# Optimization experiments

Measured on AMD Instinct MI355X. Metric: run time of the kernel, lower is better.

Reference implementation:

```python
import jax, jax.numpy as jnp
import numpy as np

D_MODEL = 1024
NHEAD = 16
HEAD_DIM = D_MODEL // NHEAD
NEG = -1e9
LN_EPS = 1e-5


def setup_inputs() -> dict:
    key = jax.random.key(0)
    ks = jax.random.split(key, 12)
    B, S, D = 2, 2048, D_MODEL
    scale = 1.0 / np.sqrt(D)
    inp = {
        "x": jax.random.normal(ks[0], (B, S, D), jnp.float32),
        "mask": jax.random.randint(ks[1], (B, S), 0, 2, jnp.int32),
        "wq": jax.random.normal(ks[2], (D, D), jnp.float32) * scale,
        "bq": jnp.zeros((D,), jnp.float32),
        "wk": jax.random.normal(ks[3], (D, D), jnp.float32) * scale,
        "bk": jnp.zeros((D,), jnp.float32),
        "wv": jax.random.normal(ks[4], (D, D), jnp.float32) * scale,
        "bv": jnp.zeros((D,), jnp.float32),
        "wo": jax.random.normal(ks[5], (D, D), jnp.float32) * scale,
        "bo": jnp.zeros((D,), jnp.float32),
        "attn_bias": jax.random.normal(ks[6], (1, NHEAD, 1, 1), jnp.float32) * 0.02,
        "ln_g": jnp.ones((D,), jnp.float32),
        "ln_b": jnp.zeros((D,), jnp.float32),
    }
    return inp


def _layer_norm(x, g, b):
    mu = jnp.mean(x, axis=-1, keepdims=True)
    var = jnp.var(x, axis=-1, keepdims=True)
    return (x - mu) * jax.lax.rsqrt(var + LN_EPS) * g + b


def reference(x, mask, wq, bq, wk, bk, wv, bv, wo, bo, attn_bias, ln_g, ln_b):
    B, S, D = x.shape
    H, Hd = NHEAD, HEAD_DIM
    # QKV projections -> [B, H, S, Hd]
    q = (x @ wq + bq).reshape(B, S, H, Hd).transpose(0, 2, 1, 3)
    k = (x @ wk + bk).reshape(B, S, H, Hd).transpose(0, 2, 1, 3)
    v = (x @ wv + bv).reshape(B, S, H, Hd).transpose(0, 2, 1, 3)
    # Scores [B, H, S, S] with per-head scalar bias
    scores = jnp.einsum("bhsd,bhtd->bhst", q, k) / jnp.sqrt(jnp.float32(Hd))
    scores = scores + attn_bias
    # mask [B,S] -> [B,1,1,S]; masked_fill where mask == 0
    m = (mask[:, None, None, :] == 0)
    scores = jnp.where(m, jnp.float32(NEG), scores)
    attn = jax.nn.softmax(scores, axis=-1)  # dropout = identity (eval)
    out = jnp.einsum("bhst,bhtd->bhsd", attn, v)
    out = out.transpose(0, 2, 1, 3).reshape(B, S, D)
    out = out @ wo + bo
    return _layer_norm(x + out, ln_g, ln_b)
```

## Files before the change

kernel.cpp:

```cpp
#include <hip/hip_runtime.h>

typedef __attribute__((ext_vector_type(8))) short short8;
typedef __attribute__((ext_vector_type(4))) float f32x4;
typedef __attribute__((ext_vector_type(16))) float f32x16;
typedef __attribute__((ext_vector_type(4))) unsigned short us4;

#define DEV __device__ __forceinline__

#define GLD16(gp, lp) __builtin_amdgcn_global_load_lds( \
    (const __attribute__((address_space(1))) void*)(gp), \
    (__attribute__((address_space(3))) void*)(lp), 16, 0, 0)

DEV unsigned short f2bf(float f) {
    union { float f; unsigned u; } v; v.f = f;
    unsigned r = v.u + 0x7fffu + ((v.u >> 16) & 1u);
    return (unsigned short)(r >> 16);
}

DEV float bf2f(unsigned short u) {
    union { unsigned u; float f; } v; v.u = (unsigned)u << 16;
    return v.f;
}

DEV unsigned short f2h(float f) {
    union { _Float16 h; unsigned short u; } v; v.h = (_Float16)f; return v.u;
}

DEV float h2f(unsigned short u) {
    union { _Float16 h; unsigned short u; } v; v.u = u; return (float)v.h;
}

DEV unsigned cvtpk(float lo, float hi) {
    unsigned r;
    asm("v_cvt_pk_bf16_f32 %0, %1, %2" : "=v"(r) : "v"(lo), "v"(hi));
    return r;
}

DEV float fexp2(float x) {
#if __has_builtin(__builtin_amdgcn_exp2f)
    return __builtin_amdgcn_exp2f(x);
#else
    return __expf(x * 0.69314718056f);
#endif
}

__global__ __launch_bounds__(256) void k_prep(const float* __restrict__ x, unsigned short* __restrict__ xb,
                                              const float* __restrict__ wq, const float* __restrict__ wk,
                                              const float* __restrict__ wv, const float* __restrict__ wo,
                                              unsigned short* __restrict__ wt) {
    __shared__ float tile[32][33];
    const int id = blockIdx.x, tid = threadIdx.x;
    if (id < 4096) {
        int i = id * 256 + tid;
        float4 v = ((const float4*)x)[i];
        us4 o = { f2bf(v.x), f2bf(v.y), f2bf(v.z), f2bf(v.w) };
        ((us4*)xb)[i] = o;
        return;
    }
    const int t = (id - 4096) & 1023, z = (id - 4096) >> 10;
    const float* src = (z == 0) ? wq : (z == 1) ? wk : (z == 2) ? wv : wo;
    unsigned short* dst = wt + (size_t)z * (1u << 20);
    const int n0 = (t & 31) * 32, k0 = (t >> 5) * 32;
    const int tx = tid & 31, ty = tid >> 5;
#pragma unroll
    for (int i = 0; i < 4; ++i)
        tile[ty + i * 8][tx] = src[(size_t)(k0 + ty + i * 8) * 1024 + n0 + tx];
    __syncthreads();
#pragma unroll
    for (int i = 0; i < 4; ++i)
        dst[(size_t)(n0 + ty + i * 8) * 1024 + k0 + tx] = f2bf(tile[tx][ty + i * 8]);
}

__global__ __launch_bounds__(256) void k_gemm_qkv(const unsigned short* __restrict__ A,
                                                  const unsigned short* __restrict__ Wt,
                                                  const float* __restrict__ bq,
                                                  const float* __restrict__ bk,
                                                  const float* __restrict__ bv,
                                                  const int* __restrict__ mask,
                                                  unsigned short* __restrict__ Qo,
                                                  unsigned short* __restrict__ Ko,
                                                  unsigned short* __restrict__ Vo,
                                                  float qscale) {
    __shared__ unsigned short lA[2][128 * 32];
    __shared__ unsigned short lB[2][3][64 * 32];
    const int id = blockIdx.x;
    const int m0 = ((id & 7) * 4 + ((id >> 3) & 3)) * 128;
    const int n0 = (id >> 5) * 64;
    const int tid = threadIdx.x;
    const int lane = tid & 63;
    const int w = tid >> 6, wm = w >> 1, wn = w & 1;

    const int arow0 = tid >> 2, acl = tid & 3;
    const int arow1 = (tid + 256) >> 2;
    const int brow = tid >> 2;
    const unsigned short* agp0 = A + (size_t)(m0 + arow0) * 1024 + acl * 8;
    const unsigned short* agp1 = A + (size_t)(m0 + arow1) * 1024 + acl * 8;
    const unsigned short* bgp[3];
#pragma unroll
    for (int z = 0; z < 3; ++z)
        bgp[z] = Wt + ((size_t)z << 20) + (size_t)(n0 + brow) * 1024 + acl * 8;
    const int apc0 = ((arow0 << 2) | (acl ^ ((arow0 >> 1) & 3))) * 8;
    const int apc1 = ((arow1 << 2) | (acl ^ ((arow1 >> 1) & 3))) * 8;
    const int bpc  = ((brow  << 2) | (acl ^ ((brow  >> 1) & 3))) * 8;

    int ach[4], bch[2];
#pragma unroll
    for (int mt = 0; mt < 4; ++mt) {
        int row = wm * 64 + mt * 16 + (lane & 15);
        ach[mt] = ((row << 2) | ((lane >> 4) ^ ((row >> 1) & 3))) * 8;
    }
#pragma unroll
    for (int nt = 0; nt < 2; ++nt) {
        int row = wn * 32 + nt * 16 + (lane & 15);
        bch[nt] = ((row << 2) | ((lane >> 4) ^ ((row >> 1) & 3))) * 8;
    }

    f32x4 acc[3][4][2] = {};
    short8 ra0 = *(const short8*)agp0;
    short8 ra1 = *(const short8*)agp1;
    short8 rb[3];
#pragma unroll
    for (int z = 0; z < 3; ++z) rb[z] = *(const short8*)bgp[z];

    for (int t = 0; t < 32; ++t) {
        unsigned short* sA = lA[t & 1];
        *(short8*)(sA + apc0) = ra0;
        *(short8*)(sA + apc1) = ra1;
#pragma unroll
        for (int z = 0; z < 3; ++z)
            *(short8*)(lB[t & 1][z] + bpc) = rb[z];
        if (t < 31) {
            ra0 = *(const short8*)(agp0 + (t + 1) * 32);
            ra1 = *(const short8*)(agp1 + (t + 1) * 32);
#pragma unroll
            for (int z = 0; z < 3; ++z) rb[z] = *(const short8*)(bgp[z] + (t + 1) * 32);
        }
        __syncthreads();
        short8 af[4], bf[3][2];
#pragma unroll
        for (int mt = 0; mt < 4; ++mt) af[mt] = *(const short8*)(sA + ach[mt]);
#pragma unroll
        for (int z = 0; z < 3; ++z)
#pragma unroll
            for (int nt = 0; nt < 2; ++nt) bf[z][nt] = *(const short8*)(lB[t & 1][z] + bch[nt]);
#pragma unroll
        for (int z = 0; z < 3; ++z)
#pragma unroll
            for (int mt = 0; mt < 4; ++mt)
#pragma unroll
                for (int nt = 0; nt < 2; ++nt)
                    acc[z][mt][nt] = __builtin_amdgcn_mfma_f32_16x16x32_bf16(af[mt], bf[z][nt], acc[z][mt][nt], 0, 0, 0);
    }

#pragma unroll
    for (int z = 0; z < 3; ++z) {
        const float* bias = (z == 0) ? bq : (z == 1) ? bk : bv;
        const float scl = (z == 0) ? qscale : 1.0f;
        unsigned short* outp = (z == 0) ? Qo : (z == 1) ? Ko : Vo;
#pragma unroll
        for (int nt = 0; nt < 2; ++nt) {
            const int col = n0 + wn * 32 + nt * 16 + (lane & 15);
            const float bvv = bias[col];
            const int h = col >> 6, hd = col & 63;
#pragma unroll
            for (int mt = 0; mt < 4; ++mt) {
#pragma unroll
                for (int r = 0; r < 4; ++r) {
                    const int row = m0 + wm * 64 + mt * 16 + (lane >> 4) * 4 + r;
                    const int b = row >> 11, s = row & 2047;
                    float v = (acc[z][mt][nt][r] + bvv) * scl;
                    if (z == 2) {
                        v *= (mask[(size_t)b * 2048 + s] ? 1.0f : 0.0f);
                        outp[(size_t)((b * 16 + h) * 64 + hd) * 2048 + s] = f2bf(v);
                    } else {
                        outp[(size_t)((b * 16 + h) * 2048 + s) * 64 + hd] = f2bf(v);
                    }
                }
            }
        }
    }
}

__global__ __launch_bounds__(256) void k_gemm_o(const unsigned short* __restrict__ A,
                                                const unsigned short* __restrict__ Wt,
                                                const float* __restrict__ bias,
                                                unsigned short* __restrict__ out) {
    __shared__ unsigned short lA[2][128 * 32];
    __shared__ unsigned short lB[2][128 * 32];
    const int id = blockIdx.x;
    const int kk = id >> 3;
    const int m0 = ((id & 7) * 4 + (kk >> 3)) * 128;
    const int n0 = (kk & 7) * 128;
    const int tid = threadIdx.x;
    const int lane = tid & 63;
    const int w = tid >> 6, wm = w >> 1, wn = w & 1;

    const int arow0 = tid >> 2, acl = tid & 3;
    const int arow1 = arow0 + 64;
    const unsigned short* agp0 = A + (size_t)(m0 + arow0) * 1024 + acl * 8;
    const unsigned short* agp1 = A + (size_t)(m0 + arow1) * 1024 + acl * 8;
    const unsigned short* bgp0 = Wt + (size_t)(n0 + arow0) * 1024 + acl * 8;
    const unsigned short* bgp1 = Wt + (size_t)(n0 + arow1) * 1024 + acl * 8;
    const int apc0 = ((arow0 << 2) | (acl ^ ((arow0 >> 1) & 3))) * 8;
    const int apc1 = ((arow1 << 2) | (acl ^ ((arow1 >> 1) & 3))) * 8;

    int ach[4], bch[4];
#pragma unroll
    for (int mt = 0; mt < 4; ++mt) {
        int row = wm * 64 + mt * 16 + (lane & 15);
        ach[mt] = ((row << 2) | ((lane >> 4) ^ ((row >> 1) & 3))) * 8;
    }
#pragma unroll
    for (int nt = 0; nt < 4; ++nt) {
        int row = wn * 64 + nt * 16 + (lane & 15);
        bch[nt] = ((row << 2) | ((lane >> 4) ^ ((row >> 1) & 3))) * 8;
    }

    f32x4 acc[4][4] = {};
    short8 ra0 = *(const short8*)agp0;
    short8 ra1 = *(const short8*)agp1;
    short8 rb0 = *(const short8*)bgp0;
    short8 rb1 = *(const short8*)bgp1;

    for (int t = 0; t < 32; ++t) {
        unsigned short* sA = lA[t & 1];
        unsigned short* sB = lB[t & 1];
        *(short8*)(sA + apc0) = ra0;
        *(short8*)(sA + apc1) = ra1;
        *(short8*)(sB + apc0) = rb0;
        *(short8*)(sB + apc1) = rb1;
        if (t < 31) {
            ra0 = *(const short8*)(agp0 + (t + 1) * 32);
            ra1 = *(const short8*)(agp1 + (t + 1) * 32);
            rb0 = *(const short8*)(bgp0 + (t + 1) * 32);
            rb1 = *(const short8*)(bgp1 + (t + 1) * 32);
        }
        __syncthreads();
        short8 af[4], bf[4];
#pragma unroll
        for (int mt = 0; mt < 4; ++mt) af[mt] = *(const short8*)(sA + ach[mt]);
#pragma unroll
        for (int nt = 0; nt < 4; ++nt) bf[nt] = *(const short8*)(sB + bch[nt]);
#pragma unroll
        for (int mt = 0; mt < 4; ++mt)
#pragma unroll
            for (int nt = 0; nt < 4; ++nt)
                acc[mt][nt] = __builtin_amdgcn_mfma_f32_16x16x32_bf16(af[mt], bf[nt], acc[mt][nt], 0, 0, 0);
    }

#pragma unroll
    for (int nt = 0; nt < 4; ++nt) {
        const int col = n0 + wn * 64 + nt * 16 + (lane & 15);
        const float bv = bias[col];
#pragma unroll
        for (int mt = 0; mt < 4; ++mt)
#pragma unroll
            for (int r = 0; r < 4; ++r) {
                const int row = m0 + wm * 64 + mt * 16 + (lane >> 4) * 4 + r;
                out[(size_t)row * 1024 + col] = f2bf(acc[mt][nt][r] + bv);
            }
    }
}

__global__ __launch_bounds__(256, 3) void k_attn(const unsigned short* __restrict__ Qb,
                                                 const unsigned short* __restrict__ Kb,
                                                 const unsigned short* __restrict__ Vt,
                                                 const int* __restrict__ mask,
                                                 unsigned short* __restrict__ po0,
                                                 unsigned short* __restrict__ po1,
                                                 unsigned short* __restrict__ po2,
                                                 unsigned short* __restrict__ po3,
                                                 float* __restrict__ lp) {
    __shared__ unsigned short ksm[3 * 4096];
    __shared__ unsigned short vsm[3 * 4096];
    __shared__ unsigned short mv[512];
    const int id = blockIdx.x;
    const int xcd = id & 7, slot = id >> 3;
    const int half = slot & 3, qt = (slot >> 2) & 15, bh = xcd * 4 + (slot >> 6);
    const int b = bh >> 4, h = bh & 15;
    const int tid = threadIdx.x, l = tid & 63, w = tid >> 6;
    const int q = l & 31, hi = l >> 5;

    {
        int2 m = ((const int2*)(mask + b * 2048 + half * 512))[tid];
        ((unsigned*)mv)[tid] = (m.x ? 0x3F80u : 0u) | ((m.y ? 0x3F80u : 0u) << 16);
    }
    asm volatile("s_waitcnt lgkmcnt(0)" ::: "memory");

    const size_t bhS = (size_t)bh * 2048;
    const unsigned short* Kbh = Kb + (bhS + half * 512) * 64;
    const unsigned short* Vbh = Vt + (size_t)bh * 64 * 2048;
    const int q0 = qt * 128 + w * 32;

    const int srow = l >> 3;
    const int sxor = 8 * ((l & 7) ^ ((l >> 3) & 7));
    const unsigned short* Ksrc = Kbh + (size_t)(w * 16 + srow) * 64 + sxor;
    const unsigned short* Vsrc = Vbh + (size_t)(w * 16 + srow) * 2048 + half * 512 + sxor;
    unsigned short* lk0 = ksm + w * 1024;
    unsigned short* lv0 = vsm + w * 1024;

#define STAGE(kt_, buf_) { \
    const unsigned short* gk = Ksrc + (size_t)(kt_) * 4096; \
    const unsigned short* gv = Vsrc + (kt_) * 64; \
    unsigned short* lk = lk0 + (buf_) * 4096; \
    unsigned short* lv = lv0 + (buf_) * 4096; \
    GLD16(gk, lk); GLD16(gk + 512, lk + 512); \
    GLD16(gv, lv); GLD16(gv + 16384, lv + 512); }

    int kro[2][4], vro[2][2][2];
#pragma unroll
    for (int sub = 0; sub < 2; ++sub) {
#pragma unroll
        for (int db = 0; db < 4; ++db) {
            int key = q + sub * 32;
            kro[sub][db] = key * 128 + ((db * 32 + hi * 16) ^ ((key & 7) << 4));
        }
#pragma unroll
        for (int kg = 0; kg < 2; ++kg)
#pragma unroll
            for (int dh = 0; dh < 2; ++dh) {
                int row = q + dh * 32;
                vro[sub][kg][dh] = row * 128 + ((sub * 64 + kg * 32 + hi * 16) ^ ((row & 7) << 4));
            }
    }

    short8 qf[4];
#pragma unroll
    for (int db = 0; db < 4; ++db)
        qf[db] = *(const short8*)(Qb + (bhS + q0 + q) * 64 + db * 16 + hi * 8);

    f32x16 o0 = {}, o1 = {}, ol = {};

    STAGE(0, 0);
    STAGE(1, 1);

#pragma unroll
    for (int kt = 0; kt < 8; ++kt) {
        const int cur = kt % 3;
        if (kt < 7) {
            asm volatile("s_waitcnt vmcnt(4)" ::: "memory");
        } else {
            asm volatile("s_waitcnt vmcnt(0)" ::: "memory");
        }
        __builtin_amdgcn_s_barrier();
        if (kt < 6) STAGE(kt + 2, (kt + 2) % 3);
        __builtin_amdgcn_sched_barrier(0);
        const char* kb = (const char*)(ksm + cur * 4096);
        const char* vb = (const char*)(vsm + cur * 4096);
#pragma unroll
        for (int sub = 0; sub < 2; ++sub) {
            short8 kf0 = *(const short8*)(kb + kro[sub][0]);
            short8 kf1 = *(const short8*)(kb + kro[sub][1]);
            short8 kf2 = *(const short8*)(kb + kro[sub][2]);
            short8 kf3 = *(const short8*)(kb + kro[sub][3]);
            f32x16 sa = {};
            __builtin_amdgcn_s_setprio(1);
            sa = __builtin_amdgcn_mfma_f32_32x32x16_bf16(kf0, qf[0], sa, 0, 0, 0);
            sa = __builtin_amdgcn_mfma_f32_32x32x16_bf16(kf1, qf[1], sa, 0, 0, 0);
            sa = __builtin_amdgcn_mfma_f32_32x32x16_bf16(kf2, qf[2], sa, 0, 0, 0);
            sa = __builtin_amdgcn_mfma_f32_32x32x16_bf16(kf3, qf[3], sa, 0, 0, 0);
            __builtin_amdgcn_s_setprio(0);
            float p[16];
#pragma unroll
            for (int r = 0; r < 16; ++r) p[r] = fexp2(sa[r]);
            union { unsigned u[4]; short8 s8; } af[2];
#pragma unroll
            for (int kg = 0; kg < 2; ++kg) {
                unsigned P0 = cvtpk(p[kg * 8 + 0], p[kg * 8 + 1]);
                unsigned P1 = cvtpk(p[kg * 8 + 2], p[kg * 8 + 3]);
                unsigned P2 = cvtpk(p[kg * 8 + 4], p[kg * 8 + 5]);
                unsigned P3 = cvtpk(p[kg * 8 + 6], p[kg * 8 + 7]);
                asm("v_permlane32_swap_b32 %0, %1" : "+v"(P0), "+v"(P2));
                asm("v_permlane32_swap_b32 %0, %1" : "+v"(P1), "+v"(P3));
                af[kg].u[0] = P0; af[kg].u[1] = P1; af[kg].u[2] = P2; af[kg].u[3] = P3;
            }
#pragma unroll
            for (int kg = 0; kg < 2; ++kg) {
                short8 vf0 = *(const short8*)(vb + vro[sub][kg][0]);
                short8 vf1 = *(const short8*)(vb + vro[sub][kg][1]);
                short8 mfr = *(const short8*)(mv + kt * 64 + sub * 32 + kg * 16 + hi * 8);
                __builtin_amdgcn_s_setprio(1);
                o0 = __builtin_amdgcn_mfma_f32_32x32x16_bf16(af[kg].s8, vf0, o0, 0, 0, 0);
                o1 = __builtin_amdgcn_mfma_f32_32x32x16_bf16(af[kg].s8, vf1, o1, 0, 0, 0);
                ol = __builtin_amdgcn_mfma_f32_32x32x16_bf16(af[kg].s8, mfr, ol, 0, 0, 0);
                __builtin_amdgcn_s_setprio(0);
            }
        }
        __builtin_amdgcn_sched_barrier(0);
    }
#undef STAGE

    float* lpx = lp + (size_t)half * 65536 + bhS;
    if (q == 0) {
#pragma unroll
        for (int r = 0; r < 16; ++r) {
            int crow = (r & 3) + 8 * (r >> 2) + 4 * hi;
            lpx[q0 + crow] = ol[r];
        }
    }
    unsigned short* pox = (half == 0) ? po0 : (half == 1) ? po1 : (half == 2) ? po2 : po3;
    unsigned short* pop = pox + ((size_t)b * 2048 + q0) * 1024 + h * 64 + q;
#pragma unroll
    for (int r = 0; r < 16; ++r) {
        int qrow = (r & 3) + 8 * (r >> 2) + 4 * hi;
        pop[(size_t)qrow * 1024] = f2h(o0[r]);
        pop[(size_t)qrow * 1024 + 32] = f2h(o1[r]);
    }
}

__global__ __launch_bounds__(256) void k_comb(const unsigned short* __restrict__ po0,
                                              const unsigned short* __restrict__ po1,
                                              const unsigned short* __restrict__ po2,
                                              const unsigned short* __restrict__ po3,
                                              const float* __restrict__ lp,
                                              unsigned short* __restrict__ ao) {
    const int idx8 = blockIdx.x * 256 + threadIdx.x;
    const int e = idx8 * 8;
    const int row = e >> 10, c = e & 1023;
    const int h = c >> 6, b = row >> 11, s = row & 2047;
    const size_t li = ((size_t)(b * 16 + h) << 11) + s;
    const float lsum = lp[li] + lp[65536 + li] + lp[2 * 65536 + li] + lp[3 * 65536 + li];
    const float rinv = __builtin_amdgcn_rcpf(lsum);
    short8 a0 = ((const short8*)po0)[idx8];
    short8 a1 = ((const short8*)po1)[idx8];
    short8 a2 = ((const short8*)po2)[idx8];
    short8 a3 = ((const short8*)po3)[idx8];
    short8 o;
#pragma unroll
    for (int j = 0; j < 8; ++j) {
        float s4 = (h2f((unsigned short)a0[j]) + h2f((unsigned short)a1[j]))
                 + (h2f((unsigned short)a2[j]) + h2f((unsigned short)a3[j]));
        o[j] = (short)f2bf(s4 * rinv);
    }
    ((short8*)ao)[idx8] = o;
}

__global__ __launch_bounds__(256) void k_ln(const float* __restrict__ x, const unsigned short* __restrict__ op,
                                            const float* __restrict__ g, const float* __restrict__ be,
                                            float* __restrict__ out) {
    const int row = blockIdx.x, tid = threadIdx.x;
    const float4 xv = ((const float4*)(x + (size_t)row * 1024))[tid];
    const us4 ov = ((const us4*)(op + (size_t)row * 1024))[tid];
    float4 v = { xv.x + bf2f(ov.x), xv.y + bf2f(ov.y), xv.z + bf2f(ov.z), xv.w + bf2f(ov.w) };
    float sum = v.x + v.y + v.z + v.w;
    float ss = v.x * v.x + v.y * v.y + v.z * v.z + v.w * v.w;
#pragma unroll
    for (int xm = 1; xm < 64; xm <<= 1) {
        sum += __shfl_xor(sum, xm, 64);
        ss += __shfl_xor(ss, xm, 64);
    }
    __shared__ float red[8];
    const int lane = tid & 63, w = tid >> 6;
    if (lane == 0) { red[w] = sum; red[4 + w] = ss; }
    __syncthreads();
    sum = red[0] + red[1] + red[2] + red[3];
    ss = red[4] + red[5] + red[6] + red[7];
    const float mu = sum * (1.0f / 1024.0f);
    const float rstd = rsqrtf(ss * (1.0f / 1024.0f) - mu * mu + 1e-5f);
    const float4 gv = ((const float4*)g)[tid];
    const float4 bv = ((const float4*)be)[tid];
    float4 o = { (v.x - mu) * rstd * gv.x + bv.x, (v.y - mu) * rstd * gv.y + bv.y,
                 (v.z - mu) * rstd * gv.z + bv.z, (v.w - mu) * rstd * gv.w + bv.w };
    ((float4*)(out + (size_t)row * 1024))[tid] = o;
}

extern "C" void kernel_launch(void* const* d_in, const int* in_sizes, int n_in,
                              void* d_out, int out_size, void* d_ws, size_t ws_size,
                              hipStream_t stream) {
    const float* x        = (const float*)d_in[0];
    const int*   mask     = (const int*)d_in[1];
    const float* wq       = (const float*)d_in[2];
    const float* bq       = (const float*)d_in[3];
    const float* wk       = (const float*)d_in[4];
    const float* bk       = (const float*)d_in[5];
    const float* wv       = (const float*)d_in[6];
    const float* bv       = (const float*)d_in[7];
    const float* wo       = (const float*)d_in[8];
    const float* bo       = (const float*)d_in[9];
    const float* ln_g     = (const float*)d_in[11];
    const float* ln_b     = (const float*)d_in[12];

    char* ws = (char*)d_ws;
    unsigned short* xb  = (unsigned short*)(ws);
    unsigned short* wt  = (unsigned short*)(ws + (8ll  << 20));
    unsigned short* qb  = (unsigned short*)(ws + (16ll << 20));
    unsigned short* kb  = (unsigned short*)(ws + (24ll << 20));
    unsigned short* vtb = (unsigned short*)(ws + (32ll << 20));
    unsigned short* po1 = (unsigned short*)(ws + (40ll << 20));
    float*          lp  = (float*)(ws + (48ll << 20));
    unsigned short* po0 = xb;
    unsigned short* po2 = (unsigned short*)d_out;
    unsigned short* po3 = po2 + (4ll << 20);
    unsigned short* ao  = qb;
    unsigned short* opj = kb;

    const float qscale = 0.125f * 1.44269504f;

    k_prep<<<8192, 256, 0, stream>>>(x, xb, wq, wk, wv, wo, wt);
    k_gemm_qkv<<<512, 256, 0, stream>>>(xb, wt, bq, bk, bv, mask, qb, kb, vtb, qscale);
    k_attn<<<2048, 256, 0, stream>>>(qb, kb, vtb, mask, po0, po1, po2, po3, lp);
    k_comb<<<2048, 256, 0, stream>>>(po0, po1, po2, po3, lp, ao);
    k_gemm_o<<<256, 256, 0, stream>>>(ao, wt + (3u << 20), bo, opj);
    k_ln<<<4096, 256, 0, stream>>>(x, opj, ln_g, ln_b, (float*)d_out);
}
```

Baseline: 130.0 us.

## Double query rows per attention wave and switch to double-buffered K/V staging

```diff
diff --git a/kernel.cpp b/kernel.cpp
--- a/kernel.cpp
+++ b/kernel.cpp
@@ -271,12 +271,12 @@
                                                  unsigned short* __restrict__ po2,
                                                  unsigned short* __restrict__ po3,
                                                  float* __restrict__ lp) {
-    __shared__ unsigned short ksm[3 * 4096];
-    __shared__ unsigned short vsm[3 * 4096];
+    __shared__ unsigned short ksm[2 * 4096];
+    __shared__ unsigned short vsm[2 * 4096];
     __shared__ unsigned short mv[512];
     const int id = blockIdx.x;
     const int xcd = id & 7, slot = id >> 3;
-    const int half = slot & 3, qt = (slot >> 2) & 15, bh = xcd * 4 + (slot >> 6);
+    const int half = slot & 3, qt = (slot >> 2) & 7, bh = xcd * 4 + (slot >> 5);
     const int b = bh >> 4, h = bh & 15;
     const int tid = threadIdx.x, l = tid & 63, w = tid >> 6;
     const int q = l & 31, hi = l >> 5;
@@ -290,7 +290,7 @@
     const size_t bhS = (size_t)bh * 2048;
     const unsigned short* Kbh = Kb + (bhS + half * 512) * 64;
     const unsigned short* Vbh = Vt + (size_t)bh * 64 * 2048;
-    const int q0 = qt * 128 + w * 32;
+    const int q0 = qt * 256 + w * 64;
 
     const int srow = l >> 3;
     const int sxor = 8 * ((l & 7) ^ ((l >> 3) & 7));
@@ -324,26 +324,26 @@
             }
     }
 
-    short8 qf[4];
-#pragma unroll
-    for (int db = 0; db < 4; ++db)
-        qf[db] = *(const short8*)(Qb + (bhS + q0 + q) * 64 + db * 16 + hi * 8);
-
-    f32x16 o0 = {}, o1 = {}, ol = {};
+    short8 qfA[4], qfB[4];
+#pragma unroll
+    for (int db = 0; db < 4; ++db) {
+        qfA[db] = *(const short8*)(Qb + (bhS + q0 + q) * 64 + db * 16 + hi * 8);
+        qfB[db] = *(const short8*)(Qb + (bhS + q0 + 32 + q) * 64 + db * 16 + hi * 8);
+    }
+
+    f32x16 o00 = {}, o01 = {}, o10 = {}, o11 = {}, ol0 = {}, ol1 = {};
 
     STAGE(0, 0);
-    STAGE(1, 1);
-
-#pragma unroll
+
     for (int kt = 0; kt < 8; ++kt) {
-        const int cur = kt % 3;
+        const int cur = kt & 1;
         if (kt < 7) {
+            STAGE(kt + 1, cur ^ 1);
             asm volatile("s_waitcnt vmcnt(4)" ::: "memory");
         } else {
             asm volatile("s_waitcnt vmcnt(0)" ::: "memory");
         }
         __builtin_amdgcn_s_barrier();
-        if (kt < 6) STAGE(kt + 2, (kt + 2) % 3);
         __builtin_amdgcn_sched_barrier(0);
         const char* kb = (const char*)(ksm + cur * 4096);
         const char* vb = (const char*)(vsm + cur * 4096);
@@ -353,26 +353,47 @@
             short8 kf1 = *(const short8*)(kb + kro[sub][1]);
             short8 kf2 = *(const short8*)(kb + kro[sub][2]);
             short8 kf3 = *(const short8*)(kb + kro[sub][3]);
-            f32x16 sa = {};
+            f32x16 sa0 = {}, sa1 = {};
             __builtin_amdgcn_s_setprio(1);
-            sa = __builtin_amdgcn_mfma_f32_32x32x16_bf16(kf0, qf[0], sa, 0, 0, 0);
-            sa = __builtin_amdgcn_mfma_f32_32x32x16_bf16(kf1, qf[1], sa, 0, 0, 0);
-            sa = __builtin_amdgcn_mfma_f32_32x32x16_bf16(kf2, qf[2], sa, 0, 0, 0);
-            sa = __builtin_amdgcn_mfma_f32_32x32x16_bf16(kf3, qf[3], sa, 0, 0, 0);
+            sa0 = __builtin_amdgcn_mfma_f32_32x32x16_bf16(kf0, qfA[0], sa0, 0, 0, 0);
+            sa1 = __builtin_amdgcn_mfma_f32_32x32x16_bf16(kf0, qfB[0], sa1, 0, 0, 0);
+            sa0 = __builtin_amdgcn_mfma_f32_32x32x16_bf16(kf1, qfA[1], sa0, 0, 0, 0);
+            sa1 = __builtin_amdgcn_mfma_f32_32x32x16_bf16(kf1, qfB[1], sa1, 0, 0, 0);
+            sa0 = __builtin_amdgcn_mfma_f32_32x32x16_bf16(kf2, qfA[2], sa0, 0, 0, 0);
+            sa1 = __builtin_amdgcn_mfma_f32_32x32x16_bf16(kf2, qfB[2], sa1, 0, 0, 0);
+            sa0 = __builtin_amdgcn_mfma_f32_32x32x16_bf16(kf3, qfA[3], sa0, 0, 0, 0);
+            sa1 = __builtin_amdgcn_mfma_f32_32x32x16_bf16(kf3, qfB[3], sa1, 0, 0, 0);
             __builtin_amdgcn_s_setprio(0);
-            float p[16];
-#pragma unroll
-            for (int r = 0; r < 16; ++r) p[r] = fexp2(sa[r]);
-            union { unsigned u[4]; short8 s8; } af[2];
-#pragma unroll
-            for (int kg = 0; kg < 2; ++kg) {
-                unsigned P0 = cvtpk(p[kg * 8 + 0], p[kg * 8 + 1]);
-                unsigned P1 = cvtpk(p[kg * 8 + 2], p[kg * 8 + 3]);
-                unsigned P2 = cvtpk(p[kg * 8 + 4], p[kg * 8 + 5]);
-                unsigned P3 = cvtpk(p[kg * 8 + 6], p[kg * 8 + 7]);
-                asm("v_permlane32_swap_b32 %0, %1" : "+v"(P0), "+v"(P2));
-                asm("v_permlane32_swap_b32 %0, %1" : "+v"(P1), "+v"(P3));
-                af[kg].u[0] = P0; af[kg].u[1] = P1; af[kg].u[2] = P2; af[kg].u[3] = P3;
+            union { unsigned u[4]; short8 s8; } afA[2], afB[2];
+            {
+                float p[16];
+#pragma unroll
+                for (int r = 0; r < 16; ++r) p[r] = fexp2(sa0[r]);
+#pragma unroll
+                for (int kg = 0; kg < 2; ++kg) {
+                    unsigned P0 = cvtpk(p[kg * 8 + 0], p[kg * 8 + 1]);
+                    unsigned P1 = cvtpk(p[kg * 8 + 2], p[kg * 8 + 3]);
+                    unsigned P2 = cvtpk(p[kg * 8 + 4], p[kg * 8 + 5]);
+                    unsigned P3 = cvtpk(p[kg * 8 + 6], p[kg * 8 + 7]);
+                    asm("v_permlane32_swap_b32 %0, %1" : "+v"(P0), "+v"(P2));
+                    asm("v_permlane32_swap_b32 %0, %1" : "+v"(P1), "+v"(P3));
+                    afA[kg].u[0] = P0; afA[kg].u[1] = P1; afA[kg].u[2] = P2; afA[kg].u[3] = P3;
+                }
+            }
+            {
+                float p[16];
+#pragma unroll
+                for (int r = 0; r < 16; ++r) p[r] = fexp2(sa1[r]);
+#pragma unroll
+                for (int kg = 0; kg < 2; ++kg) {
+                    unsigned P0 = cvtpk(p[kg * 8 + 0], p[kg * 8 + 1]);
+                    unsigned P1 = cvtpk(p[kg * 8 + 2], p[kg * 8 + 3]);
+                    unsigned P2 = cvtpk(p[kg * 8 + 4], p[kg * 8 + 5]);
+                    unsigned P3 = cvtpk(p[kg * 8 + 6], p[kg * 8 + 7]);
+                    asm("v_permlane32_swap_b32 %0, %1" : "+v"(P0), "+v"(P2));
+                    asm("v_permlane32_swap_b32 %0, %1" : "+v"(P1), "+v"(P3));
+                    afB[kg].u[0] = P0; afB[kg].u[1] = P1; afB[kg].u[2] = P2; afB[kg].u[3] = P3;
+                }
             }
 #pragma unroll
             for (int kg = 0; kg < 2; ++kg) {
@@ -380,13 +401,17 @@
                 short8 vf1 = *(const short8*)(vb + vro[sub][kg][1]);
                 short8 mfr = *(const short8*)(mv + kt * 64 + sub * 32 + kg * 16 + hi * 8);
                 __builtin_amdgcn_s_setprio(1);
-                o0 = __builtin_amdgcn_mfma_f32_32x32x16_bf16(af[kg].s8, vf0, o0, 0, 0, 0);
-                o1 = __builtin_amdgcn_mfma_f32_32x32x16_bf16(af[kg].s8, vf1, o1, 0, 0, 0);
-                ol = __builtin_amdgcn_mfma_f32_32x32x16_bf16(af[kg].s8, mfr, ol, 0, 0, 0);
+                o00 = __builtin_amdgcn_mfma_f32_32x32x16_bf16(afA[kg].s8, vf0, o00, 0, 0, 0);
+                o01 = __builtin_amdgcn_mfma_f32_32x32x16_bf16(afA[kg].s8, vf1, o01, 0, 0, 0);
+                o10 = __builtin_amdgcn_mfma_f32_32x32x16_bf16(afB[kg].s8, vf0, o10, 0, 0, 0);
+                o11 = __builtin_amdgcn_mfma_f32_32x32x16_bf16(afB[kg].s8, vf1, o11, 0, 0, 0);
+                ol0 = __builtin_amdgcn_mfma_f32_32x32x16_bf16(afA[kg].s8, mfr, ol0, 0, 0, 0);
+                ol1 = __builtin_amdgcn_mfma_f32_32x32x16_bf16(afB[kg].s8, mfr, ol1, 0, 0, 0);
                 __builtin_amdgcn_s_setprio(0);
             }
         }
         __builtin_amdgcn_sched_barrier(0);
+        if (kt < 7) __builtin_amdgcn_s_barrier();
     }
 #undef STAGE
 
@@ -395,16 +420,20 @@
 #pragma unroll
         for (int r = 0; r < 16; ++r) {
             int crow = (r & 3) + 8 * (r >> 2) + 4 * hi;
-            lpx[q0 + crow] = ol[r];
+            lpx[q0 + crow] = ol0[r];
+            lpx[q0 + 32 + crow] = ol1[r];
         }
     }
     unsigned short* pox = (half == 0) ? po0 : (half == 1) ? po1 : (half == 2) ? po2 : po3;
-    unsigned short* pop = pox + ((size_t)b * 2048 + q0) * 1024 + h * 64 + q;
+    unsigned short* popA = pox + ((size_t)b * 2048 + q0) * 1024 + h * 64 + q;
+    unsigned short* popB = popA + (size_t)32 * 1024;
 #pragma unroll
     for (int r = 0; r < 16; ++r) {
         int qrow = (r & 3) + 8 * (r >> 2) + 4 * hi;
-        pop[(size_t)qrow * 1024] = f2h(o0[r]);
-        pop[(size_t)qrow * 1024 + 32] = f2h(o1[r]);
+        popA[(size_t)qrow * 1024] = f2h(o00[r]);
+        popA[(size_t)qrow * 1024 + 32] = f2h(o01[r]);
+        popB[(size_t)qrow * 1024] = f2h(o10[r]);
+        popB[(size_t)qrow * 1024 + 32] = f2h(o11[r]);
     }
 }
 
@@ -498,7 +527,7 @@
 
     k_prep<<<8192, 256, 0, stream>>>(x, xb, wq, wk, wv, wo, wt);
     k_gemm_qkv<<<512, 256, 0, stream>>>(xb, wt, bq, bk, bv, mask, qb, kb, vtb, qscale);
-    k_attn<<<2048, 256, 0, stream>>>(qb, kb, vtb, mask, po0, po1, po2, po3, lp);
+    k_attn<<<1024, 256, 0, stream>>>(qb, kb, vtb, mask, po0, po1, po2, po3, lp);
     k_comb<<<2048, 256, 0, stream>>>(po0, po1, po2, po3, lp, ao);
     k_gemm_o<<<256, 256, 0, stream>>>(ao, wt + (3u << 20), bo, opj);
     k_ln<<<4096, 256, 0, stream>>>(x, opj, ln_g, ln_b, (float*)d_out);
```

Measured after the change: 176.4 us. 1.36x slower.
